# Performance work log

Hardware: AMD Instinct MI355X
Metric: run time of the kernel (lower is better)

Reference implementation:

```python
import jax, jax.numpy as jnp
import numpy as np

N_EMBD = 1024
N_HEAD = 16
HEAD_DIM = N_EMBD // N_HEAD
LN_EPS = 1e-5


def setup_inputs() -> dict:
    key = jax.random.key(0)
    ks = jax.random.split(key, 8)
    B, T, C = 4, 2048, N_EMBD
    s = lambda fan_in: 1.0 / np.sqrt(fan_in)
    return {
        'x': jax.random.normal(ks[0], (B, T, C), dtype=jnp.float32),
        'w_qkv': jax.random.normal(ks[1], (C, 3 * C), dtype=jnp.float32) * s(C),
        'b_qkv': jnp.zeros((3 * C,), dtype=jnp.float32),
        'ln1_g': jnp.ones((C,), dtype=jnp.float32),
        'ln1_b': jnp.zeros((C,), dtype=jnp.float32),
        'w_fc1': jax.random.normal(ks[2], (C, 4 * C), dtype=jnp.float32) * s(C),
        'b_fc1': jnp.zeros((4 * C,), dtype=jnp.float32),
        'w_fc2': jax.random.normal(ks[3], (4 * C, C), dtype=jnp.float32) * s(4 * C),
        'b_fc2': jnp.zeros((C,), dtype=jnp.float32),
        'ln2_g': jnp.ones((C,), dtype=jnp.float32),
        'ln2_b': jnp.zeros((C,), dtype=jnp.float32),
    }


def _layernorm(x, g, b):
    mu = jnp.mean(x, axis=-1, keepdims=True)
    var = jnp.mean(jnp.square(x - mu), axis=-1, keepdims=True)
    return (x - mu) * jax.lax.rsqrt(var + LN_EPS) * g + b


def _attention(x, w_qkv, b_qkv):
    B, T, C = x.shape
    qkv = x @ w_qkv + b_qkv                      # [B,T,3C]
    q, k, v = jnp.split(qkv, 3, axis=-1)
    q = q.reshape(B, T, N_HEAD, HEAD_DIM)
    k = k.reshape(B, T, N_HEAD, HEAD_DIM)
    v = v.reshape(B, T, N_HEAD, HEAD_DIM)
    scores = jnp.einsum('bqhd,bkhd->bhqk', q, k) / np.sqrt(HEAD_DIM).astype(np.float32)
    causal = jnp.tril(jnp.ones((T, T), dtype=bool))
    scores = jnp.where(causal, scores, -jnp.inf)
    attn = jax.nn.softmax(scores, axis=-1)       # [B,H,T,T]
    y = jnp.einsum('bhqk,bkhd->bqhd', attn, v)
    return y.reshape(B, T, C)


def reference(x, w_qkv, b_qkv, ln1_g, ln1_b, w_fc1, b_fc1, w_fc2, b_fc2, ln2_g, ln2_b):
    # Block: x = ln1(x + attn(x)); x = ln2(x + mlp(x))   (post-LN residual)
    x = _layernorm(x + _attention(x, w_qkv, b_qkv), ln1_g, ln1_b)
    h = jax.nn.gelu(x @ w_fc1 + b_fc1, approximate=False)
    mlp = h @ w_fc2 + b_fc2
    x = _layernorm(x + mlp, ln2_g, ln2_b)
    return x
```

## Files before the change

kernel.cpp:

```cpp
#include <hip/hip_runtime.h>
#include <cstdint>
#include <cstddef>

#define TB 4
#define TT 2048
#define TC 1024
#define NH 16
#define HD 64
#define MROWS (TB * TT)

typedef __bf16 bf16;
typedef unsigned short u16;
typedef __bf16 bf16x8 __attribute__((ext_vector_type(8)));
typedef float floatx4 __attribute__((ext_vector_type(4)));
typedef unsigned short ushort8 __attribute__((ext_vector_type(8)));
typedef unsigned short ushort4v __attribute__((ext_vector_type(4)));

#define LOG2E 1.4426950408889634f

static __device__ __forceinline__ u16 f2bfbits(float f) {
    bf16 b = (bf16)f;
    return __builtin_bit_cast(u16, b);
}

#if __has_builtin(__builtin_amdgcn_exp2f)
#define EXP2F(x) __builtin_amdgcn_exp2f(x)
#else
#define EXP2F(x) exp2f(x)
#endif

static __device__ __forceinline__ void gld_lds16(const u16* g, const u16* lds) {
    __builtin_amdgcn_global_load_lds(
        (const __attribute__((address_space(1))) unsigned int*)(uintptr_t)g,
        (__attribute__((address_space(3))) unsigned int*)(unsigned int)(uintptr_t)lds,
        16, 0, 0);
}

__global__ __launch_bounds__(256) void prep_kernel(
    const float* __restrict__ x, u16* __restrict__ xb,
    const float* __restrict__ w_qkv, u16* __restrict__ wqkvT,
    const float* __restrict__ w_fc1, u16* __restrict__ wfc1T,
    const float* __restrict__ w_fc2, u16* __restrict__ wfc2T)
{
    const int tid = threadIdx.x;
    int blk = blockIdx.x;
    if (blk < 8192) {
        const int i = blk * 256 + tid;
        float4 v = reinterpret_cast<const float4*>(x)[i];
        ushort4v o;
        o.x = f2bfbits(v.x); o.y = f2bfbits(v.y); o.z = f2bfbits(v.z); o.w = f2bfbits(v.w);
        reinterpret_cast<ushort4v*>(xb)[i] = o;
        return;
    }
    blk -= 8192;
    const float* in; u16* out; int K, N, bx, by;
    if (blk < 3072)      { in = w_qkv; out = wqkvT; K = TC;     N = 3 * TC; bx = blk % 96;  by = blk / 96; }
    else if (blk < 7168) { blk -= 3072; in = w_fc1; out = wfc1T; K = TC;    N = 4 * TC; bx = blk & 127; by = blk >> 7; }
    else                 { blk -= 7168; in = w_fc2; out = wfc2T; K = 4 * TC; N = TC;    bx = blk & 31;  by = blk >> 5; }
    __shared__ float tile[32][33];
    const int n0 = bx * 32, k0 = by * 32;
    const int tx = tid & 31, ty = tid >> 5;
    for (int r = 0; r < 32; r += 8)
        tile[ty + r][tx] = in[(size_t)(k0 + ty + r) * N + n0 + tx];
    __syncthreads();
    for (int r = 0; r < 32; r += 8)
        out[(size_t)(n0 + ty + r) * K + k0 + tx] = f2bfbits(tile[tx][ty + r]);
}

template <int GELU>
__global__ __launch_bounds__(256) void gemm_bt_kernel(
    const u16* __restrict__ A, const u16* __restrict__ Bt,
    const float* __restrict__ bias, u16* __restrict__ Cmat,
    int Nsz, int Ksz)
{
    __shared__ u16 As[128 * 64];
    __shared__ u16 Bs[128 * 64];
    const int tid  = threadIdx.x;
    const int wave = tid >> 6, lane = tid & 63;
    const int quad = lane >> 4, l16 = lane & 15;
    const int wm = (wave >> 1) * 64, wn = (wave & 1) * 64;
    const int m0 = blockIdx.y * 128, n0 = blockIdx.x * 128;

    const int srow = lane >> 3;
    const int scol = ((lane & 7) ^ srow) * 8;
    const u16* ap = A  + (size_t)(m0 + wave * 32 + srow) * Ksz + scol;
    const u16* bp = Bt + (size_t)(n0 + wave * 32 + srow) * Ksz + scol;
    const size_t dstep = (size_t)8 * Ksz;

    floatx4 acc[4][4];
#pragma unroll
    for (int i = 0; i < 4; i++)
#pragma unroll
        for (int j = 0; j < 4; j++)
            acc[i][j] = (floatx4){0.f, 0.f, 0.f, 0.f};

    const int l7 = l16 & 7;

    for (int k0 = 0; k0 < Ksz; k0 += 64) {
        __syncthreads();
#pragma unroll
        for (int d = 0; d < 4; d++) {
            gld_lds16(ap + d * dstep, As + (wave * 4 + d) * 512);
            gld_lds16(bp + d * dstep, Bs + (wave * 4 + d) * 512);
        }
        ap += 64; bp += 64;
        __syncthreads();

#pragma unroll
        for (int t = 0; t < 2; t++) {
            const int po = ((t * 4 + quad) ^ l7) * 8;
            bf16x8 af[4], bfr[4];
#pragma unroll
            for (int i = 0; i < 4; i++)
                af[i] = *reinterpret_cast<const bf16x8*>(As + (wm + i * 16 + l16) * 64 + po);
#pragma unroll
            for (int j = 0; j < 4; j++)
                bfr[j] = *reinterpret_cast<const bf16x8*>(Bs + (wn + j * 16 + l16) * 64 + po);
#pragma unroll
            for (int i = 0; i < 4; i++)
#pragma unroll
                for (int j = 0; j < 4; j++)
                    acc[i][j] = __builtin_amdgcn_mfma_f32_16x16x32_bf16(af[i], bfr[j], acc[i][j], 0, 0, 0);
        }
    }

    float bv[4];
#pragma unroll
    for (int j = 0; j < 4; j++) bv[j] = bias[n0 + wn + j * 16 + l16];
    const int odd = l16 & 1;
#pragma unroll
    for (int i = 0; i < 4; i++) {
        const int row0 = m0 + wm + i * 16 + quad * 4;
#pragma unroll
        for (int j = 0; j < 4; j++) {
            float v[4];
#pragma unroll
            for (int r = 0; r < 4; r++) {
                float t = acc[i][j][r] + bv[j];
                if (GELU) {
                    float u = t * (0.7978845608f + 0.0356774081f * t * t);
                    float e = EXP2F(u * (2.0f * LOG2E));
                    t = t - t * __builtin_amdgcn_rcpf(e + 1.0f);
                }
                v[r] = t;
            }
            float pv0 = __shfl_xor(v[0], 1), pv1 = __shfl_xor(v[1], 1);
            float pv2 = __shfl_xor(v[2], 1), pv3 = __shfl_xor(v[3], 1);
            float lo0 = odd ? pv2 : v[0];
            float hi0 = odd ? v[2] : pv0;
            float lo1 = odd ? pv3 : v[1];
            float hi1 = odd ? v[3] : pv1;
            unsigned int d0 = (unsigned int)f2bfbits(lo0) | ((unsigned int)f2bfbits(hi0) << 16);
            unsigned int d1 = (unsigned int)f2bfbits(lo1) | ((unsigned int)f2bfbits(hi1) << 16);
            const int row  = row0 + odd * 2;
            const int colp = n0 + wn + j * 16 + (l16 & ~1);
            *reinterpret_cast<unsigned int*>(Cmat + (size_t)row * Nsz + colp)       = d0;
            *reinterpret_cast<unsigned int*>(Cmat + (size_t)(row + 1) * Nsz + colp) = d1;
        }
    }
}

__global__ __launch_bounds__(512) void attn_kernel(const u16* __restrict__ qkv,
                                                   u16* __restrict__ y)
{
    __shared__ u16 Ks[2 * 64 * 64];
    __shared__ u16 Vt[2 * 64 * 64];
    __shared__ u16 Pw[8][16 * 64];
    const int tid  = threadIdx.x;
    const int wave = tid >> 6, lane = tid & 63;
    const int quad = lane >> 4, l16 = lane & 15;
    const int l7   = l16 & 7;
    const int h = blockIdx.y, b = blockIdx.z;
    const int rowbase = b * TT;
    const int S3C = 3 * TC;

    const int srow = (tid >> 3) & 31;
    const int c8   = (tid & 7) * 8;
    const int pcK  = ((tid & 7) ^ (srow & 7)) * 8;
    const int pvb  = (srow + ((tid & 7) << 2)) & 31;
    const bool kRole = (tid < 256);
    const int pcr = (quad ^ l7) * 8;
    unsigned int* const vtw = (unsigned int*)Vt;

    for (int pass = 0; pass < 2; pass++) {
        const int qt   = pass ? (15 - (int)blockIdx.x) : (int)blockIdx.x;
        const int q0b  = qt * 128;
        const int q0w  = q0b + wave * 16;
        const int kend = q0b + 128;

        __syncthreads();

        bf16x8 qf0, qf1;
        {
            const u16* qrow = qkv + (size_t)(rowbase + q0w + l16) * S3C + h * HD + quad * 8;
            bf16x8 t0 = *reinterpret_cast<const bf16x8*>(qrow);
            bf16x8 t1 = *reinterpret_cast<const bf16x8*>(qrow + 32);
#pragma unroll
            for (int i = 0; i < 8; i++) {
                t0[i] = (bf16)((float)t0[i] * (0.125f * LOG2E));
                t1[i] = (bf16)((float)t1[i] * (0.125f * LOG2E));
            }
            qf0 = t0; qf1 = t1;
        }

        float m_s = -__builtin_inff(), l_s = 0.f;
        floatx4 o_acc[4];
#pragma unroll
        for (int n = 0; n < 4; n++) o_acc[n] = (floatx4){0.f, 0.f, 0.f, 0.f};

        const u16* gp = kRole
            ? qkv + (size_t)(rowbase + srow) * S3C + TC + h * HD + c8
            : qkv + (size_t)(rowbase + 2 * srow) * S3C + 2 * TC + h * HD + c8;
        const size_t g2 = kRole ? (size_t)32 * S3C : (size_t)S3C;
        ushort8 r0 = *reinterpret_cast<const ushort8*>(gp);
        ushort8 r1 = *reinterpret_cast<const ushort8*>(gp + g2);

        int buf = 0;
        for (int k0 = 0; k0 < kend; k0 += 64) {
            if (kRole) {
                u16* kb = Ks + buf * 4096;
                *reinterpret_cast<ushort8*>(kb + srow * 64 + pcK)        = r0;
                *reinterpret_cast<ushort8*>(kb + (srow + 32) * 64 + pcK) = r1;
            } else {
                unsigned int* vb = vtw + buf * 2048;
#pragma unroll
                for (int j = 0; j < 8; j++) {
                    unsigned int pk = (unsigned int)r0[j] | ((unsigned int)r1[j] << 16);
                    vb[(c8 + j) * 32 + (pvb ^ (j << 2))] = pk;
                }
            }
            __syncthreads();

            if (k0 + 64 < kend) {
                const u16* gn = gp + (size_t)(k0 + 64) * S3C;
                r0 = *reinterpret_cast<const ushort8*>(gn);
                r1 = *reinterpret_cast<const ushort8*>(gn + g2);
            }

            if (k0 <= q0w + 15) {
                const u16* ksb = Ks + buf * 4096;
                floatx4 st[4];
#pragma unroll
                for (int t = 0; t < 4; t++) {
                    const u16* krowp = ksb + (t * 16 + l16) * 64;
                    bf16x8 ka  = *reinterpret_cast<const bf16x8*>(krowp + pcr);
                    bf16x8 kb2 = *reinterpret_cast<const bf16x8*>(krowp + (pcr ^ 32));
                    floatx4 s = (floatx4){0.f, 0.f, 0.f, 0.f};
                    s = __builtin_amdgcn_mfma_f32_16x16x32_bf16(ka, qf0, s, 0, 0, 0);
                    s = __builtin_amdgcn_mfma_f32_16x16x32_bf16(kb2, qf1, s, 0, 0, 0);
                    st[t] = s;
                }
                float v[16];
                if (k0 + 63 > q0w) {
                    const int kq = k0 - q0w;
#pragma unroll
                    for (int t = 0; t < 4; t++)
#pragma unroll
                        for (int r = 0; r < 4; r++)
                            v[t * 4 + r] = (t * 16 + quad * 4 + r + kq > l16)
                                               ? -__builtin_inff() : st[t][r];
                } else {
#pragma unroll
                    for (int t = 0; t < 4; t++)
#pragma unroll
                        for (int r = 0; r < 4; r++)
                            v[t * 4 + r] = st[t][r];
                }
                float mx = v[0];
#pragma unroll
                for (int i = 1; i < 16; i++) mx = fmaxf(mx, v[i]);
                mx = fmaxf(mx, __shfl_xor(mx, 16));
                mx = fmaxf(mx, __shfl_xor(mx, 32));
                const float mnew  = fmaxf(m_s, mx);
                const float alpha = EXP2F(m_s - mnew);
                float rs = 0.f;
                u16* const pwb = Pw[wave] + l16 * 64;
#pragma unroll
                for (int t = 0; t < 4; t++) {
                    float p0 = EXP2F(v[t * 4 + 0] - mnew);
                    float p1 = EXP2F(v[t * 4 + 1] - mnew);
                    float p2 = EXP2F(v[t * 4 + 2] - mnew);
                    float p3 = EXP2F(v[t * 4 + 3] - mnew);
                    rs += (p0 + p1) + (p2 + p3);
                    ushort4v pk;
                    pk.x = f2bfbits(p0); pk.y = f2bfbits(p1);
                    pk.z = f2bfbits(p2); pk.w = f2bfbits(p3);
                    *reinterpret_cast<ushort4v*>(
                        pwb + ((2 * t + (quad >> 1)) ^ l7) * 8 + (quad & 1) * 4) = pk;
                }
                rs += __shfl_xor(rs, 16);
                rs += __shfl_xor(rs, 32);
                l_s = l_s * alpha + rs;
                m_s = mnew;
#pragma unroll
                for (int n = 0; n < 4; n++) o_acc[n] *= alpha;

                bf16x8 pf0 = *reinterpret_cast<const bf16x8*>(pwb + pcr);
                bf16x8 pf1 = *reinterpret_cast<const bf16x8*>(pwb + (pcr ^ 32));
                const unsigned int* vbb = vtw + buf * 2048;
#pragma unroll
                for (int n = 0; n < 4; n++) {
                    const int dr  = n * 16 + l16;
                    const int pd0 = ((4 * (quad + 2 * n + (l16 >> 3))) & 31) ^ (l7 << 2);
                    bf16x8 vf0 = *reinterpret_cast<const bf16x8*>(vbb + dr * 32 + pd0);
                    bf16x8 vf1 = *reinterpret_cast<const bf16x8*>(vbb + dr * 32 + (pd0 ^ 16));
                    o_acc[n] = __builtin_amdgcn_mfma_f32_16x16x32_bf16(vf0, pf0, o_acc[n], 0, 0, 0);
                    o_acc[n] = __builtin_amdgcn_mfma_f32_16x16x32_bf16(vf1, pf1, o_acc[n], 0, 0, 0);
                }
            }
            buf ^= 1;
        }

        const float li = 1.0f / l_s;
        u16* yrow = y + (size_t)(rowbase + q0w + l16) * TC + h * HD;
#pragma unroll
        for (int n = 0; n < 4; n++) {
            ushort4v ov;
            ov.x = f2bfbits(o_acc[n][0] * li);
            ov.y = f2bfbits(o_acc[n][1] * li);
            ov.z = f2bfbits(o_acc[n][2] * li);
            ov.w = f2bfbits(o_acc[n][3] * li);
            *reinterpret_cast<ushort4v*>(yrow + n * 16 + quad * 4) = ov;
        }
    }
}

template <typename AT, typename OT>
__global__ __launch_bounds__(256) void ln_kernel(
    const AT* __restrict__ a, const bf16* __restrict__ bres,
    const float* __restrict__ g, const float* __restrict__ be,
    OT* __restrict__ out)
{
    const int row = blockIdx.x;
    const int tid = threadIdx.x;
    const size_t base = (size_t)row * TC;
    float v[4];
    for (int i = 0; i < 4; i++) {
        const int c = tid + i * 256;
        v[i] = (float)a[base + c] + (float)bres[base + c];
    }
    float s  = v[0] + v[1] + v[2] + v[3];
    float sq = v[0]*v[0] + v[1]*v[1] + v[2]*v[2] + v[3]*v[3];
    for (int off = 32; off >= 1; off >>= 1) {
        s  += __shfl_xor(s, off, 64);
        sq += __shfl_xor(sq, off, 64);
    }
    __shared__ float red[8];
    const int wv = tid >> 6, lane = tid & 63;
    if (lane == 0) { red[wv] = s; red[4 + wv] = sq; }
    __syncthreads();
    s  = red[0] + red[1] + red[2] + red[3];
    sq = red[4] + red[5] + red[6] + red[7];
    const float mu   = s * (1.0f / TC);
    const float var  = sq * (1.0f / TC) - mu * mu;
    const float rsig = rsqrtf(var + 1e-5f);
    for (int i = 0; i < 4; i++) {
        const int c = tid + i * 256;
        out[base + c] = (OT)((v[i] - mu) * rsig * g[c] + be[c]);
    }
}

extern "C" void kernel_launch(void* const* d_in, const int* in_sizes, int n_in,
                              void* d_out, int out_size, void* d_ws, size_t ws_size,
                              hipStream_t stream)
{
    const float* x     = (const float*)d_in[0];
    const float* w_qkv = (const float*)d_in[1];
    const float* b_qkv = (const float*)d_in[2];
    const float* ln1_g = (const float*)d_in[3];
    const float* ln1_b = (const float*)d_in[4];
    const float* w_fc1 = (const float*)d_in[5];
    const float* b_fc1 = (const float*)d_in[6];
    const float* w_fc2 = (const float*)d_in[7];
    const float* b_fc2 = (const float*)d_in[8];
    const float* ln2_g = (const float*)d_in[9];
    const float* ln2_b = (const float*)d_in[10];
    float* out = (float*)d_out;

    char* ws = (char*)d_ws;
    const size_t MB = 1ull << 20;
    u16* xb    = (u16*)(ws + 0);
    u16* wqkvT = (u16*)(ws + 16 * MB);
    u16* wfc1T = (u16*)(ws + 22 * MB);
    u16* wfc2T = (u16*)(ws + 30 * MB);
    u16* qkv   = (u16*)(ws + 38 * MB);
    u16* yb    = (u16*)(ws + 86 * MB);
    u16* x1    = (u16*)(ws + 102 * MB);
    u16* hb    = (u16*)(ws + 118 * MB);
    u16* mlp   = (u16*)(ws + 38 * MB);

    prep_kernel<<<19456, 256, 0, stream>>>(x, xb, w_qkv, wqkvT, w_fc1, wfc1T, w_fc2, wfc2T);

    gemm_bt_kernel<0><<<dim3(3 * TC / 128, MROWS / 128), 256, 0, stream>>>(
        xb, wqkvT, b_qkv, qkv, 3 * TC, TC);
    attn_kernel<<<dim3(8, NH, TB), 512, 0, stream>>>(qkv, yb);
    ln_kernel<float, bf16><<<MROWS, 256, 0, stream>>>(x, (const bf16*)yb, ln1_g, ln1_b, (bf16*)x1);
    gemm_bt_kernel<1><<<dim3(4 * TC / 128, MROWS / 128), 256, 0, stream>>>(
        (const u16*)x1, wfc1T, b_fc1, hb, 4 * TC, TC);
    gemm_bt_kernel<0><<<dim3(TC / 128, MROWS / 128), 256, 0, stream>>>(
        hb, wfc2T, b_fc2, mlp, TC, 4 * TC);
    ln_kernel<bf16, float><<<MROWS, 256, 0, stream>>>(
        (const bf16*)x1, (const bf16*)mlp, ln2_g, ln2_b, out);
}
```

Measured before the change: 465.4 us.

## Widen GEMM tiles to 128x256 with XCD-aware block-to-tile mapping

Each GEMM block now computes a 128x256 output tile instead of 128x128, doubling per-wave accumulators to 4x8 MFMA tiles for more reuse of each A fragment loaded from LDS. The grid becomes 1-D, and block IDs are remapped so that consecutive blocks landing on the same XCD share an M-row band, aiming to improve L2 locality for A and B. Launch bounds request 2 blocks per CU. The cost is higher register pressure (128 accumulator floats per lane) and fewer, larger blocks; the FC2 GEMM drops to only 256 blocks, which may underfill the GPU.

```diff
diff --git a/kernel.cpp b/kernel.cpp
--- a/kernel.cpp
+++ b/kernel.cpp
@@ -68,30 +68,35 @@
 }
 
 template <int GELU>
-__global__ __launch_bounds__(256) void gemm_bt_kernel(
+__global__ __launch_bounds__(256, 2) void gemm_bt_kernel(
     const u16* __restrict__ A, const u16* __restrict__ Bt,
     const float* __restrict__ bias, u16* __restrict__ Cmat,
-    int Nsz, int Ksz)
+    int Nb, int Ksz)
 {
     __shared__ u16 As[128 * 64];
-    __shared__ u16 Bs[128 * 64];
+    __shared__ u16 Bs[256 * 64];
     const int tid  = threadIdx.x;
     const int wave = tid >> 6, lane = tid & 63;
     const int quad = lane >> 4, l16 = lane & 15;
-    const int wm = (wave >> 1) * 64, wn = (wave & 1) * 64;
-    const int m0 = blockIdx.y * 128, n0 = blockIdx.x * 128;
+    const int Nsz = Nb * 256;
+    const int bid = blockIdx.x;
+    const int xcd = bid & 7, qb = bid >> 3;
+    const int m0 = (xcd * 8 + qb / Nb) * 128;
+    const int n0 = (qb % Nb) * 256;
+    const int wm = (wave >> 1) * 64, wn = (wave & 1) * 128;
 
     const int srow = lane >> 3;
     const int scol = ((lane & 7) ^ srow) * 8;
     const u16* ap = A  + (size_t)(m0 + wave * 32 + srow) * Ksz + scol;
-    const u16* bp = Bt + (size_t)(n0 + wave * 32 + srow) * Ksz + scol;
-    const size_t dstep = (size_t)8 * Ksz;
-
-    floatx4 acc[4][4];
+    const u16* bp = Bt + (size_t)(n0 + wave * 8  + srow) * Ksz + scol;
+    const size_t astep = (size_t)8  * Ksz;
+    const size_t bstep = (size_t)32 * Ksz;
+
+    floatx4 acc[4][8];
 #pragma unroll
     for (int i = 0; i < 4; i++)
 #pragma unroll
-        for (int j = 0; j < 4; j++)
+        for (int j = 0; j < 8; j++)
             acc[i][j] = (floatx4){0.f, 0.f, 0.f, 0.f};
 
     const int l7 = l16 & 7;
@@ -99,40 +104,41 @@
     for (int k0 = 0; k0 < Ksz; k0 += 64) {
         __syncthreads();
 #pragma unroll
-        for (int d = 0; d < 4; d++) {
-            gld_lds16(ap + d * dstep, As + (wave * 4 + d) * 512);
-            gld_lds16(bp + d * dstep, Bs + (wave * 4 + d) * 512);
-        }
+        for (int d = 0; d < 4; d++)
+            gld_lds16(ap + d * astep, As + (wave * 4 + d) * 512);
+#pragma unroll
+        for (int d = 0; d < 8; d++)
+            gld_lds16(bp + d * bstep, Bs + d * 2048 + wave * 512);
         ap += 64; bp += 64;
         __syncthreads();
 
 #pragma unroll
         for (int t = 0; t < 2; t++) {
             const int po = ((t * 4 + quad) ^ l7) * 8;
-            bf16x8 af[4], bfr[4];
+            bf16x8 af[4], bfr[8];
 #pragma unroll
             for (int i = 0; i < 4; i++)
                 af[i] = *reinterpret_cast<const bf16x8*>(As + (wm + i * 16 + l16) * 64 + po);
 #pragma unroll
-            for (int j = 0; j < 4; j++)
+            for (int j = 0; j < 8; j++)
                 bfr[j] = *reinterpret_cast<const bf16x8*>(Bs + (wn + j * 16 + l16) * 64 + po);
 #pragma unroll
             for (int i = 0; i < 4; i++)
 #pragma unroll
-                for (int j = 0; j < 4; j++)
+                for (int j = 0; j < 8; j++)
                     acc[i][j] = __builtin_amdgcn_mfma_f32_16x16x32_bf16(af[i], bfr[j], acc[i][j], 0, 0, 0);
         }
     }
 
-    float bv[4];
-#pragma unroll
-    for (int j = 0; j < 4; j++) bv[j] = bias[n0 + wn + j * 16 + l16];
+    float bv[8];
+#pragma unroll
+    for (int j = 0; j < 8; j++) bv[j] = bias[n0 + wn + j * 16 + l16];
     const int odd = l16 & 1;
 #pragma unroll
     for (int i = 0; i < 4; i++) {
         const int row0 = m0 + wm + i * 16 + quad * 4;
 #pragma unroll
-        for (int j = 0; j < 4; j++) {
+        for (int j = 0; j < 8; j++) {
             float v[4];
 #pragma unroll
             for (int r = 0; r < 4; r++) {
@@ -391,14 +397,11 @@
 
     prep_kernel<<<19456, 256, 0, stream>>>(x, xb, w_qkv, wqkvT, w_fc1, wfc1T, w_fc2, wfc2T);
 
-    gemm_bt_kernel<0><<<dim3(3 * TC / 128, MROWS / 128), 256, 0, stream>>>(
-        xb, wqkvT, b_qkv, qkv, 3 * TC, TC);
+    gemm_bt_kernel<0><<<12 * 64, 256, 0, stream>>>(xb, wqkvT, b_qkv, qkv, 12, TC);
     attn_kernel<<<dim3(8, NH, TB), 512, 0, stream>>>(qkv, yb);
     ln_kernel<float, bf16><<<MROWS, 256, 0, stream>>>(x, (const bf16*)yb, ln1_g, ln1_b, (bf16*)x1);
-    gemm_bt_kernel<1><<<dim3(4 * TC / 128, MROWS / 128), 256, 0, stream>>>(
-        (const u16*)x1, wfc1T, b_fc1, hb, 4 * TC, TC);
-    gemm_bt_kernel<0><<<dim3(TC / 128, MROWS / 128), 256, 0, stream>>>(
-        hb, wfc2T, b_fc2, mlp, TC, 4 * TC);
+    gemm_bt_kernel<1><<<16 * 64, 256, 0, stream>>>((const u16*)x1, wfc1T, b_fc1, hb, 16, TC);
+    gemm_bt_kernel<0><<<4 * 64, 256, 0, stream>>>(hb, wfc2T, b_fc2, mlp, 4, 4 * TC);
     ln_kernel<bf16, float><<<MROWS, 256, 0, stream>>>(
         (const bf16*)x1, (const bf16*)mlp, ln2_g, ln2_b, out);
 }
```

After: 455.1 us. 1.02x faster.
